# Optimization experiments

Measured on AMD Instinct MI355X. Metric: run time of the kernel, lower is better.

Reference implementation:

```python
import math
import jax, jax.numpy as jnp
import numpy as np

B, S, E, H = 4, 2048, 1024, 16
D = E // H


def setup_inputs() -> dict:
    key = jax.random.key(0)
    k1, k2, k3 = jax.random.split(key, 3)
    return {
        "hidden_state": jax.random.normal(k1, (B, S, E), dtype=jnp.float32),
        "attention_mask": jnp.zeros((B, 1, 1, S), dtype=jnp.float32),
        "W_attn": jax.random.normal(k2, (E, 3 * E), dtype=jnp.float32) * 0.02,
        "b_attn": jnp.zeros((3 * E,), dtype=jnp.float32),
        "W_proj": jax.random.normal(k3, (E, E), dtype=jnp.float32) * 0.02,
        "b_proj": jnp.zeros((E,), dtype=jnp.float32),
    }


def reference(hidden_state, attention_mask, W_attn, b_attn, W_proj, b_proj):
    b, s, e = hidden_state.shape
    d = e // H
    # c_attn (HF Conv1D): x @ W + b -> [B,S,3E]
    x = hidden_state @ W_attn + b_attn
    q, k, v = jnp.split(x, 3, axis=-1)
    # split heads -> [B,H,S,D]
    q = q.reshape(b, s, H, d).transpose(0, 2, 1, 3)
    k = k.reshape(b, s, H, d).transpose(0, 2, 1, 3)
    v = v.reshape(b, s, H, d).transpose(0, 2, 1, 3)
    # scores [B,H,S,S]; scale=True divides by sqrt(d_head)
    w = jnp.einsum("bhqd,bhkd->bhqk", q, k) / math.sqrt(d)
    causal = jnp.tril(jnp.ones((s, s), dtype=w.dtype))[None, None]
    w = w * causal + (-10000.0) * (1.0 - causal)
    w = w + attention_mask
    w = jax.nn.softmax(w, axis=-1)  # attn_dropout p=0 (eval)
    out = jnp.einsum("bhqk,bhkd->bhqd", w, v)
    # merge heads -> [B,S,E]
    out = out.transpose(0, 2, 1, 3).reshape(b, s, e)
    # c_proj; resid_dropout p=0 (eval)
    return out @ W_proj + b_proj
```

## Files before the change

kernel.cpp:

```cpp
#include <hip/hip_runtime.h>
#include <hip/hip_bf16.h>

typedef __attribute__((ext_vector_type(4))) float f32x4;
typedef __attribute__((ext_vector_type(8))) short bf16x8;

#define B_SZ  4
#define S_LEN 2048
#define EMB   1024
#define NH    16
#define DH    64
#define E3    3072
#define QKLD  2048
#define LOG2E 1.4426950408889634f
#define SC2   (0.125f * LOG2E)
#define MSTAT 14.0f

#define VMCNT(N) asm volatile("s_waitcnt vmcnt(" #N ")" ::: "memory")
#define RAWBAR() asm volatile("s_barrier" ::: "memory")

__device__ __forceinline__ void gload_lds16(const void* g, void* l) {
  __builtin_amdgcn_global_load_lds((const __attribute__((address_space(1))) void*)g,
                                   (__attribute__((address_space(3))) void*)l, 16, 0, 0);
}

__device__ __forceinline__ float bf2f(unsigned short u) {
  union { unsigned int i; float f; } c;
  c.i = (unsigned int)u << 16;
  return c.f;
}

__device__ __forceinline__ unsigned pack_bf16_rtz(float hi, float lo) {
  union { float f; unsigned u; } a, b;
  a.f = hi; b.f = lo;
  return (a.u & 0xffff0000u) | (b.u >> 16);
}

__global__ void cvt_bf16_kernel(const float* __restrict__ in,
                                __hip_bfloat16* __restrict__ out, int n) {
  const int i = (blockIdx.x * 256 + threadIdx.x) * 4;
  if (i >= n) return;
  const float4 v = *(const float4*)(in + i);
  __align__(8) __hip_bfloat16 o[4];
  o[0] = __float2bfloat16(v.x); o[1] = __float2bfloat16(v.y);
  o[2] = __float2bfloat16(v.z); o[3] = __float2bfloat16(v.w);
  *(uint2*)(out + i) = *(const uint2*)o;
}

__global__ __launch_bounds__(256)
void transpose_cvt(const float* __restrict__ in, __hip_bfloat16* __restrict__ out,
                   int R, int C) {
  __shared__ float tile[32][33];
  const int tx = threadIdx.x & 31, ty = threadIdx.x >> 5;
  const int c = blockIdx.x * 32 + tx;
#pragma unroll
  for (int i = 0; i < 32; i += 8)
    tile[ty + i][tx] = in[(size_t)(blockIdx.y * 32 + ty + i) * C + c];
  __syncthreads();
  const int r2 = blockIdx.y * 32 + tx;
#pragma unroll
  for (int i = 0; i < 32; i += 8)
    out[(size_t)(blockIdx.x * 32 + ty + i) * R + r2] = __float2bfloat16(tile[tx][ty + i]);
}

template <int EPI>
__global__ __launch_bounds__(256, 2)
void gemm_v4(const __hip_bfloat16* __restrict__ A, const __hip_bfloat16* __restrict__ BT,
             const float* __restrict__ bias, void* __restrict__ Cout,
             __hip_bfloat16* __restrict__ vt) {
  __shared__ __attribute__((aligned(16))) char lds[73728];
  const int tid = threadIdx.x;
  const int lane = tid & 63, w = tid >> 6;
  const int lr = lane & 15, lg = lane >> 4, lg4 = lg * 4;
  const int wm = w >> 1, wn = w & 1;

  const int j = blockIdx.x;
  const int g = (j & 7) * ((int)gridDim.x >> 3) + (j >> 3);
  const int bx = g & 63, by = g >> 6;
  const int m0 = bx * 128, n0 = by * 256;

  const int ar1 = tid >> 2;
  const int ar2 = ar1 + 64;
  const int cg = tid & 3;
  const int ac1 = (cg ^ ((ar1 >> 1) & 3)) * 8;
  const int ac2 = (cg ^ ((ar2 >> 1) & 3)) * 8;
  const __hip_bfloat16* pa1 = A + (size_t)(m0 + ar1) * 1024 + ac1;
  const __hip_bfloat16* pa2 = A + (size_t)(m0 + ar2) * 1024 + ac2;
  const int br0 = tid >> 2, br1 = br0 + 64, br2 = br0 + 128, br3 = br0 + 192;
  const __hip_bfloat16* pb0 = BT + (size_t)(n0 + br0) * 1024 + (cg ^ ((br0 >> 1) & 3)) * 8;
  const __hip_bfloat16* pb1 = BT + (size_t)(n0 + br1) * 1024 + (cg ^ ((br1 >> 1) & 3)) * 8;
  const __hip_bfloat16* pb2 = BT + (size_t)(n0 + br2) * 1024 + (cg ^ ((br2 >> 1) & 3)) * 8;
  const __hip_bfloat16* pb3 = BT + (size_t)(n0 + br3) * 1024 + (cg ^ ((br3 >> 1) & 3)) * 8;
  char* const dA1 = lds + tid * 16;
  char* const dA2 = lds + 4096 + tid * 16;
  char* const dB0 = lds + 8192 + tid * 16;
  char* const dB1 = lds + 8192 + 4096 + tid * 16;
  char* const dB2 = lds + 8192 + 8192 + tid * 16;
  char* const dB3 = lds + 8192 + 12288 + tid * 16;

#define STG_V4(BUF, T) { \
    const int off_ = (T) * 32; \
    gload_lds16(pa1 + off_, dA1 + (BUF) * 24576); \
    gload_lds16(pa2 + off_, dA2 + (BUF) * 24576); \
    gload_lds16(pb0 + off_, dB0 + (BUF) * 24576); \
    gload_lds16(pb1 + off_, dB1 + (BUF) * 24576); \
    gload_lds16(pb2 + off_, dB2 + (BUF) * 24576); \
    gload_lds16(pb3 + off_, dB3 + (BUF) * 24576); }

  const int sw = (lg ^ ((lr >> 1) & 3)) << 4;
  const int abyte = (wm * 64 + lr) * 64 + sw;
  const int bbyte = 8192 + (wn * 128 + lr) * 64 + sw;

  f32x4 acc[4][8] = {};

  STG_V4(0, 0); STG_V4(1, 1);

  int cur = 0;
#pragma unroll 1
  for (int t = 0; t < 32; ++t) {
    if (t < 31) { VMCNT(6); } else { VMCNT(0); }
    RAWBAR();
    if (t + 2 < 32) {
      const int nb = (cur >= 1) ? cur - 1 : 2;
      STG_V4(nb, t + 2);
    }
    const char* base = lds + cur * 24576;
    bf16x8 a[4], b[8];
#pragma unroll
    for (int m = 0; m < 4; ++m) a[m] = *(const bf16x8*)(base + abyte + m * 1024);
#pragma unroll
    for (int n = 0; n < 8; ++n) b[n] = *(const bf16x8*)(base + bbyte + n * 1024);
#pragma unroll
    for (int m = 0; m < 4; ++m)
#pragma unroll
      for (int n = 0; n < 8; ++n)
        acc[m][n] = __builtin_amdgcn_mfma_f32_16x16x32_bf16(a[m], b[n], acc[m][n], 0, 0, 0);
    cur = (cur == 2) ? 0 : cur + 1;
  }

  if (EPI == 0 && n0 >= 2 * EMB) {
#pragma unroll
    for (int m = 0; m < 4; ++m) {
      const int rowg0 = m0 + wm * 64 + m * 16 + lg4;
      const int bz = rowg0 >> 11, sloc = rowg0 & (S_LEN - 1);
#pragma unroll
      for (int n = 0; n < 8; ++n) {
        const int col = n0 + wn * 128 + n * 16 + lr;
        const int c2 = col - 2 * EMB;
        const int hh = c2 >> 6, dd = c2 & 63;
        const float bv = bias[col];
        __align__(8) __hip_bfloat16 pb[4];
#pragma unroll
        for (int r = 0; r < 4; ++r) pb[r] = __float2bfloat16(acc[m][n][r] + bv);
        *(uint2*)&vt[(size_t)((bz * NH + hh) * DH + dd) * S_LEN + sloc] = *(const uint2*)pb;
      }
    }
  } else if (EPI == 0) {
#pragma unroll
    for (int m = 0; m < 4; ++m) {
#pragma unroll
      for (int n = 0; n < 8; ++n) {
        const int col = n0 + wn * 128 + n * 16 + lr;
        const float bv = bias[col];
#pragma unroll
        for (int r = 0; r < 4; ++r) {
          const int rowg = m0 + wm * 64 + m * 16 + lg4 + r;
          ((__hip_bfloat16*)Cout)[(size_t)rowg * QKLD + col] = __float2bfloat16(acc[m][n][r] + bv);
        }
      }
    }
  } else {
#pragma unroll
    for (int m = 0; m < 4; ++m) {
#pragma unroll
      for (int n = 0; n < 8; ++n) {
        const int col = n0 + wn * 128 + n * 16 + lr;
        const float bv = bias[col];
#pragma unroll
        for (int r = 0; r < 4; ++r) {
          const int rowg = m0 + wm * 64 + m * 16 + lg4 + r;
          ((float*)Cout)[(size_t)rowg * EMB + col] = acc[m][n][r] + bv;
        }
      }
    }
  }
#undef STG_V4
}

template <bool DIAG>
__device__ __forceinline__ void qstep(const char* Ks, const char* Vs,
                                      __hip_bfloat16 (*Psw)[72], const __hip_bfloat16* Msb,
                                      int msoff, const bf16x8 (&aq)[2], f32x4 (&acc)[4],
                                      float& lrun, int lr, int lg, int lg4, int wq) {
  f32x4 sacc[4] = {};
  __builtin_amdgcn_s_setprio(1);
#pragma unroll
  for (int kt = 0; kt < 4; ++kt)
#pragma unroll
    for (int ks = 0; ks < 2; ++ks) {
      const bf16x8 kb = *(const bf16x8*)(Ks + (kt * 16 + lr) * 128 +
                                         (((ks * 4 + lg) ^ (lr & 7)) << 4));
      sacc[kt] = __builtin_amdgcn_mfma_f32_16x16x32_bf16(kb, aq[ks], sacc[kt], 0, 0, 0);
    }
  __builtin_amdgcn_s_setprio(0);
#pragma unroll
  for (int kt = 0; kt < 4; ++kt) {
    const ushort4 mb = *(const ushort4*)&Msb[msoff + kt * 16 + lg4];
    float pp[4];
#pragma unroll
    for (int r = 0; r < 4; ++r) {
      float sv = sacc[kt][r] * SC2 + bf2f(((const unsigned short*)&mb)[r]);
      if (DIAG && (kt * 16 + lg4 + r > wq)) sv = -1.0e9f;
      pp[r] = __builtin_amdgcn_exp2f(sv);
    }
    lrun += (pp[0] + pp[1]) + (pp[2] + pp[3]);
    uint2 uu;
    uu.x = pack_bf16_rtz(pp[1], pp[0]);
    uu.y = pack_bf16_rtz(pp[3], pp[2]);
    *(uint2*)&Psw[lr][kt * 16 + lg4] = uu;
  }
#pragma unroll
  for (int ks = 0; ks < 2; ++ks) {
    const bf16x8 pa = *(const bf16x8*)&Psw[lr][ks * 32 + lg * 8];
    __builtin_amdgcn_s_setprio(1);
#pragma unroll
    for (int dt = 0; dt < 4; ++dt) {
      const bf16x8 vb = *(const bf16x8*)(Vs + (dt * 16 + lr) * 128 +
                                         (((ks * 4 + lg) ^ (lr & 7)) << 4));
      acc[dt] = __builtin_amdgcn_mfma_f32_16x16x32_bf16(pa, vb, acc[dt], 0, 0, 0);
    }
    __builtin_amdgcn_s_setprio(0);
  }
}

template <bool DIAGA>
__device__ __forceinline__ void qstep2(const char* Ks, const char* Vs,
                                       __hip_bfloat16 (*PsA)[72], __hip_bfloat16 (*PsB)[72],
                                       const __hip_bfloat16* Msb, int msoff,
                                       const bf16x8 (&aqA)[2], const bf16x8 (&aqB)[2],
                                       f32x4 (&accA)[4], f32x4 (&accB)[4],
                                       float& lA, float& lB, int lr, int lg, int lg4, int wq) {
  f32x4 sA[4] = {}, sB[4] = {};
  __builtin_amdgcn_s_setprio(1);
#pragma unroll
  for (int kt = 0; kt < 4; ++kt)
#pragma unroll
    for (int ks = 0; ks < 2; ++ks) {
      const bf16x8 kb = *(const bf16x8*)(Ks + (kt * 16 + lr) * 128 +
                                         (((ks * 4 + lg) ^ (lr & 7)) << 4));
      sA[kt] = __builtin_amdgcn_mfma_f32_16x16x32_bf16(kb, aqA[ks], sA[kt], 0, 0, 0);
      sB[kt] = __builtin_amdgcn_mfma_f32_16x16x32_bf16(kb, aqB[ks], sB[kt], 0, 0, 0);
    }
  __builtin_amdgcn_s_setprio(0);
#pragma unroll
  for (int kt = 0; kt < 4; ++kt) {
    const ushort4 mb = *(const ushort4*)&Msb[msoff + kt * 16 + lg4];
    float pA[4], pB[4];
#pragma unroll
    for (int r = 0; r < 4; ++r) {
      const float mkr = bf2f(((const unsigned short*)&mb)[r]);
      float svA = sA[kt][r] * SC2 + mkr;
      if (DIAGA && (kt * 16 + lg4 + r > wq)) svA = -1.0e9f;
      const float svB = sB[kt][r] * SC2 + mkr;
      pA[r] = __builtin_amdgcn_exp2f(svA);
      pB[r] = __builtin_amdgcn_exp2f(svB);
    }
    lA += (pA[0] + pA[1]) + (pA[2] + pA[3]);
    lB += (pB[0] + pB[1]) + (pB[2] + pB[3]);
    uint2 ua, ub;
    ua.x = pack_bf16_rtz(pA[1], pA[0]);
    ua.y = pack_bf16_rtz(pA[3], pA[2]);
    ub.x = pack_bf16_rtz(pB[1], pB[0]);
    ub.y = pack_bf16_rtz(pB[3], pB[2]);
    *(uint2*)&PsA[lr][kt * 16 + lg4] = ua;
    *(uint2*)&PsB[lr][kt * 16 + lg4] = ub;
  }
#pragma unroll
  for (int ks = 0; ks < 2; ++ks) {
    const bf16x8 paA = *(const bf16x8*)&PsA[lr][ks * 32 + lg * 8];
    const bf16x8 paB = *(const bf16x8*)&PsB[lr][ks * 32 + lg * 8];
    __builtin_amdgcn_s_setprio(1);
#pragma unroll
    for (int dt = 0; dt < 4; ++dt) {
      const bf16x8 vb = *(const bf16x8*)(Vs + (dt * 16 + lr) * 128 +
                                         (((ks * 4 + lg) ^ (lr & 7)) << 4));
      accA[dt] = __builtin_amdgcn_mfma_f32_16x16x32_bf16(paA, vb, accA[dt], 0, 0, 0);
      accB[dt] = __builtin_amdgcn_mfma_f32_16x16x32_bf16(paB, vb, accB[dt], 0, 0, 0);
    }
    __builtin_amdgcn_s_setprio(0);
  }
}

#define STAGE_LOAD_BUMP()                                                          \
  {                                                                                \
    kpre[0] = *(const bf16x8*)kcur;                                                \
    kpre[1] = *(const bf16x8*)(kcur + 8 * QKLD);                                   \
    vpre[0] = *(const bf16x8*)vcur;                                                \
    vpre[1] = *(const bf16x8*)(vcur + 8 * S_LEN);                                  \
    kcur += 64 * QKLD;                                                             \
    vcur += 64;                                                                    \
  }

#define TILE_SYNC(PREFETCH)                                                        \
  {                                                                                \
    __syncthreads();                                                               \
    *(bf16x8*)kw0 = kpre[0];                                                       \
    *(bf16x8*)(kw0 + 1024) = kpre[1];                                              \
    *(bf16x8*)vw0 = vpre[0];                                                       \
    *(bf16x8*)(vw0 + 1024) = vpre[1];                                              \
    __syncthreads();                                                               \
    if (PREFETCH) STAGE_LOAD_BUMP();                                               \
  }

__global__ __launch_bounds__(256, 4)
void flash_attn10(const __hip_bfloat16* __restrict__ qk, const __hip_bfloat16* __restrict__ vt,
                  const float* __restrict__ amask, __hip_bfloat16* __restrict__ aout) {
  const int j = blockIdx.x;
  const int g = (j & 7) + 8 * (j >> 7);
  const int x = (((j >> 3) & 15) + (((j >> 8) & 3) << 2)) & 15;
  const int h = g >> 2, bz = g & 3;

  const int tid = threadIdx.x;
  const int lane = tid & 63, w = tid >> 6;
  const int lr = lane & 15, lg = lane >> 4, lg4 = lg * 4;
  const int wq = w * 16 + lr;

  const int qta = x, qtb = 31 - x;

  __shared__ __align__(16) __hip_bfloat16 Ks[64 * 64];
  __shared__ __align__(16) __hip_bfloat16 Vs[64 * 64];
  __shared__ __align__(16) __hip_bfloat16 Ps[4][2][16][72];
  __shared__ __align__(8)  __hip_bfloat16 Msb[S_LEN];

  {
    const int e = tid * 8;
    const f32x4 m0v = *(const f32x4*)&amask[bz * S_LEN + e];
    const f32x4 m1v = *(const f32x4*)&amask[bz * S_LEN + e + 4];
    __align__(16) __hip_bfloat16 mb[8];
#pragma unroll
    for (int jj = 0; jj < 4; ++jj) {
      mb[jj]     = __float2bfloat16(m0v[jj] * LOG2E - MSTAT);
      mb[jj + 4] = __float2bfloat16(m1v[jj] * LOG2E - MSTAT);
    }
    *(uint4*)&Msb[e] = *(const uint4*)mb;
  }

  bf16x8 aqA[2], aqB[2];
  {
    const __hip_bfloat16* qpA =
        qk + (size_t)(bz * S_LEN + qta * 64 + w * 16 + lr) * QKLD + h * DH + lg * 8;
    aqA[0] = *(const bf16x8*)qpA; aqA[1] = *(const bf16x8*)(qpA + 32);
    const __hip_bfloat16* qpB =
        qk + (size_t)(bz * S_LEN + qtb * 64 + w * 16 + lr) * QKLD + h * DH + lg * 8;
    aqB[0] = *(const bf16x8*)qpB; aqB[1] = *(const bf16x8*)(qpB + 32);
  }

  f32x4 accA[4] = {}, accB[4] = {};
  float lA = 0.f, lB = 0.f;

  const __hip_bfloat16* kcur = qk + (size_t)bz * S_LEN * QKLD + EMB + h * DH +
                               (size_t)(w * 16 + (lane >> 3)) * QKLD + (lane & 7) * 8;
  const __hip_bfloat16* vcur = vt + (size_t)((bz * NH + h) * DH + w * 16 + (lane >> 3)) * S_LEN +
                               (lane & 7) * 8;
  char* kw0 = (char*)Ks + (w * 16 + (lane >> 3)) * 128 + (((lane & 7) ^ (lane >> 3)) << 4);
  char* vw0 = (char*)Vs + (w * 16 + (lane >> 3)) * 128 + (((lane & 7) ^ (lane >> 3)) << 4);

  bf16x8 kpre[2], vpre[2];
  STAGE_LOAD_BUMP();

  int msoff = 0;
  for (int t = 0; t < qta; ++t) {
    TILE_SYNC(true);
    qstep2<false>((char*)Ks, (char*)Vs, Ps[w][0], Ps[w][1], Msb, msoff,
                  aqA, aqB, accA, accB, lA, lB, lr, lg, lg4, wq);
    msoff += 64;
  }
  TILE_SYNC(true);
  qstep2<true>((char*)Ks, (char*)Vs, Ps[w][0], Ps[w][1], Msb, msoff,
               aqA, aqB, accA, accB, lA, lB, lr, lg, lg4, wq);
  msoff += 64;
  for (int t = qta + 1; t < qtb; ++t) {
    TILE_SYNC(true);
    qstep<false>((char*)Ks, (char*)Vs, Ps[w][1], Msb, msoff, aqB, accB, lB, lr, lg, lg4, wq);
    msoff += 64;
  }
  TILE_SYNC(false);
  qstep<true>((char*)Ks, (char*)Vs, Ps[w][1], Msb, msoff, aqB, accB, lB, lr, lg, lg4, wq);

  lA += __shfl_xor(lA, 16); lA += __shfl_xor(lA, 32);
  lB += __shfl_xor(lB, 16); lB += __shfl_xor(lB, 32);
  float lqA[4], lqB[4];
#pragma unroll
  for (int r = 0; r < 4; ++r) {
    lqA[r] = __shfl(lA, lg4 + r);
    lqB[r] = __shfl(lB, lg4 + r);
  }
#pragma unroll
  for (int dt = 0; dt < 4; ++dt)
#pragma unroll
    for (int r = 0; r < 4; ++r) {
      const int qA = qta * 64 + w * 16 + lg4 + r;
      aout[(size_t)(bz * S_LEN + qA) * EMB + h * DH + dt * 16 + lr] =
          __float2bfloat16(accA[dt][r] / lqA[r]);
      const int qB = qtb * 64 + w * 16 + lg4 + r;
      aout[(size_t)(bz * S_LEN + qB) * EMB + h * DH + dt * 16 + lr] =
          __float2bfloat16(accB[dt][r] / lqB[r]);
    }
}

extern "C" void kernel_launch(void* const* d_in, const int* in_sizes, int n_in,
                              void* d_out, int out_size, void* d_ws, size_t ws_size,
                              hipStream_t stream) {
  const float* hidden = (const float*)d_in[0];
  const float* amask  = (const float*)d_in[1];
  const float* W_attn = (const float*)d_in[2];
  const float* b_attn = (const float*)d_in[3];
  const float* W_proj = (const float*)d_in[4];
  const float* b_proj = (const float*)d_in[5];
  float* out = (float*)d_out;

  char* ws = (char*)d_ws;
  __hip_bfloat16* hbf   = (__hip_bfloat16*)(ws);
  __hip_bfloat16* WaT   = (__hip_bfloat16*)(ws + 16777216);
  __hip_bfloat16* WpT   = (__hip_bfloat16*)(ws + 23068672);
  __hip_bfloat16* qkQK  = (__hip_bfloat16*)(ws + 25165824);
  __hip_bfloat16* vt    = (__hip_bfloat16*)(ws + 58720256);
  __hip_bfloat16* aoutb = (__hip_bfloat16*)(ws + 75497472);

  cvt_bf16_kernel<<<dim3(8192), dim3(256), 0, stream>>>(hidden, hbf, B_SZ * S_LEN * EMB);
  transpose_cvt<<<dim3(96, 32), dim3(256), 0, stream>>>(W_attn, WaT, EMB, E3);
  transpose_cvt<<<dim3(32, 32), dim3(256), 0, stream>>>(W_proj, WpT, EMB, EMB);
  gemm_v4<0><<<dim3(768), dim3(256), 0, stream>>>(hbf, WaT, b_attn, qkQK, vt);
  flash_attn10<<<dim3(1024), dim3(256), 0, stream>>>(qkQK, vt, amask, aoutb);
  gemm_v4<1><<<dim3(256), dim3(256), 0, stream>>>(aoutb, WpT, b_proj, out, nullptr);
}
```

Measured before the change: 172.8 us.

## Use 128x384 tiles with double-buffered pipeline for QKV projection GEMM

Splits the templated GEMM into a dedicated QKV kernel and a projection kernel. The QKV kernel moves from 128x256 tiles (768 blocks, triple-buffered, two stages in flight) to 128x384 tiles (512 blocks, double-buffered, one stage in flight with a full vmcnt(0) wait each iteration). Each block now writes both the QK rows and the transposed V output per column tile. Larger tiles raise arithmetic intensity and shrink the grid to a multiple of the CU count, but they use more accumulator registers (48 f32x4 per thread) and the shallower prefetch exposes more load latency.

```diff
diff --git a/kernel.cpp b/kernel.cpp
--- a/kernel.cpp
+++ b/kernel.cpp
@@ -62,11 +62,93 @@
     out[(size_t)(blockIdx.x * 32 + ty + i) * R + r2] = __float2bfloat16(tile[tx][ty + i]);
 }
 
-template <int EPI>
 __global__ __launch_bounds__(256, 2)
-void gemm_v4(const __hip_bfloat16* __restrict__ A, const __hip_bfloat16* __restrict__ BT,
-             const float* __restrict__ bias, void* __restrict__ Cout,
-             __hip_bfloat16* __restrict__ vt) {
+void gemm_qkv_v5(const __hip_bfloat16* __restrict__ A, const __hip_bfloat16* __restrict__ BT,
+                 const float* __restrict__ bias, __hip_bfloat16* __restrict__ qkOut,
+                 __hip_bfloat16* __restrict__ vt) {
+  __shared__ __attribute__((aligned(16))) char lds[65536];
+  const int tid = threadIdx.x;
+  const int lane = tid & 63, w = tid >> 6;
+  const int lr = lane & 15, lg = lane >> 4, lg4 = lg * 4;
+  const int wm = w >> 1, wn = w & 1;
+
+  const int j = blockIdx.x;
+  const int g = (j & 7) * 64 + (j >> 3);
+  const int m0 = (g >> 3) * 128;
+  const int n0 = (g & 7) * 384;
+
+  const int r0 = tid >> 2, cg = tid & 3;
+  const int sc = (cg ^ ((r0 >> 1) & 3)) * 8;
+  const __hip_bfloat16* pA0 = A + (size_t)(m0 + r0) * 1024 + sc;
+  const __hip_bfloat16* pB0 = BT + (size_t)(n0 + r0) * 1024 + sc;
+  char* const dst = lds + tid * 16;
+
+#define STG5(B, T) { \
+    const int o_ = (T) * 32; \
+    gload_lds16(pA0 + o_,           dst + (B) * 32768); \
+    gload_lds16(pA0 + 65536 + o_,   dst + (B) * 32768 + 4096); \
+    _Pragma("unroll") \
+    for (int i_ = 0; i_ < 6; ++i_) \
+      gload_lds16(pB0 + i_ * 65536 + o_, dst + (B) * 32768 + 8192 + i_ * 4096); }
+
+  const int sw = (lg ^ ((lr >> 1) & 3)) << 4;
+  const int abyte = (wm * 64 + lr) * 64 + sw;
+  const int bbyte = 8192 + (wn * 192 + lr) * 64 + sw;
+
+  f32x4 acc[4][12] = {};
+
+  STG5(0, 0);
+  VMCNT(0);
+  RAWBAR();
+
+  int cur = 0;
+#pragma unroll 1
+  for (int t = 0; t < 32; ++t) {
+    if (t < 31) STG5(cur ^ 1, t + 1);
+    const char* base = lds + cur * 32768;
+    bf16x8 a[4], b[12];
+#pragma unroll
+    for (int m = 0; m < 4; ++m) a[m] = *(const bf16x8*)(base + abyte + m * 1024);
+#pragma unroll
+    for (int n = 0; n < 12; ++n) b[n] = *(const bf16x8*)(base + bbyte + n * 1024);
+#pragma unroll
+    for (int m = 0; m < 4; ++m)
+#pragma unroll
+      for (int n = 0; n < 12; ++n)
+        acc[m][n] = __builtin_amdgcn_mfma_f32_16x16x32_bf16(a[m], b[n], acc[m][n], 0, 0, 0);
+    if (t < 31) { VMCNT(0); RAWBAR(); }
+    cur ^= 1;
+  }
+
+#pragma unroll
+  for (int m = 0; m < 4; ++m) {
+    const int rowg0 = m0 + wm * 64 + m * 16 + lg4;
+    const int bz = rowg0 >> 11, sloc = rowg0 & (S_LEN - 1);
+#pragma unroll
+    for (int n = 0; n < 12; ++n) {
+      const int colb = n0 + wn * 192 + n * 16;
+      const int col = colb + lr;
+      const float bv = bias[col];
+      if (colb < 2 * EMB) {
+#pragma unroll
+        for (int r = 0; r < 4; ++r)
+          qkOut[(size_t)(rowg0 + r) * QKLD + col] = __float2bfloat16(acc[m][n][r] + bv);
+      } else {
+        const int c2 = col - 2 * EMB;
+        const int hh = c2 >> 6, dd = c2 & 63;
+        __align__(8) __hip_bfloat16 pb[4];
+#pragma unroll
+        for (int r = 0; r < 4; ++r) pb[r] = __float2bfloat16(acc[m][n][r] + bv);
+        *(uint2*)&vt[(size_t)((bz * NH + hh) * DH + dd) * S_LEN + sloc] = *(const uint2*)pb;
+      }
+    }
+  }
+#undef STG5
+}
+
+__global__ __launch_bounds__(256, 2)
+void gemm_proj_v4(const __hip_bfloat16* __restrict__ A, const __hip_bfloat16* __restrict__ BT,
+                  const float* __restrict__ bias, float* __restrict__ Cout) {
   __shared__ __attribute__((aligned(16))) char lds[73728];
   const int tid = threadIdx.x;
   const int lane = tid & 63, w = tid >> 6;
@@ -82,29 +164,20 @@
   const int ar2 = ar1 + 64;
   const int cg = tid & 3;
   const int ac1 = (cg ^ ((ar1 >> 1) & 3)) * 8;
-  const int ac2 = (cg ^ ((ar2 >> 1) & 3)) * 8;
   const __hip_bfloat16* pa1 = A + (size_t)(m0 + ar1) * 1024 + ac1;
-  const __hip_bfloat16* pa2 = A + (size_t)(m0 + ar2) * 1024 + ac2;
-  const int br0 = tid >> 2, br1 = br0 + 64, br2 = br0 + 128, br3 = br0 + 192;
-  const __hip_bfloat16* pb0 = BT + (size_t)(n0 + br0) * 1024 + (cg ^ ((br0 >> 1) & 3)) * 8;
-  const __hip_bfloat16* pb1 = BT + (size_t)(n0 + br1) * 1024 + (cg ^ ((br1 >> 1) & 3)) * 8;
-  const __hip_bfloat16* pb2 = BT + (size_t)(n0 + br2) * 1024 + (cg ^ ((br2 >> 1) & 3)) * 8;
-  const __hip_bfloat16* pb3 = BT + (size_t)(n0 + br3) * 1024 + (cg ^ ((br3 >> 1) & 3)) * 8;
+  const __hip_bfloat16* pa2 = A + (size_t)(m0 + ar2) * 1024 + ac1;
+  const __hip_bfloat16* pb0 = BT + (size_t)(n0 + ar1) * 1024 + ac1;
   char* const dA1 = lds + tid * 16;
   char* const dA2 = lds + 4096 + tid * 16;
   char* const dB0 = lds + 8192 + tid * 16;
-  char* const dB1 = lds + 8192 + 4096 + tid * 16;
-  char* const dB2 = lds + 8192 + 8192 + tid * 16;
-  char* const dB3 = lds + 8192 + 12288 + tid * 16;
-
-#define STG_V4(BUF, T) { \
+
+#define STG_P(BUF, T) { \
     const int off_ = (T) * 32; \
     gload_lds16(pa1 + off_, dA1 + (BUF) * 24576); \
     gload_lds16(pa2 + off_, dA2 + (BUF) * 24576); \
-    gload_lds16(pb0 + off_, dB0 + (BUF) * 24576); \
-    gload_lds16(pb1 + off_, dB1 + (BUF) * 24576); \
-    gload_lds16(pb2 + off_, dB2 + (BUF) * 24576); \
-    gload_lds16(pb3 + off_, dB3 + (BUF) * 24576); }
+    _Pragma("unroll") \
+    for (int i_ = 0; i_ < 4; ++i_) \
+      gload_lds16(pb0 + i_ * 65536 + off_, dB0 + (BUF) * 24576 + i_ * 4096); }
 
   const int sw = (lg ^ ((lr >> 1) & 3)) << 4;
   const int abyte = (wm * 64 + lr) * 64 + sw;
@@ -112,7 +185,7 @@
 
   f32x4 acc[4][8] = {};
 
-  STG_V4(0, 0); STG_V4(1, 1);
+  STG_P(0, 0); STG_P(1, 1);
 
   int cur = 0;
 #pragma unroll 1
@@ -121,7 +194,7 @@
     RAWBAR();
     if (t + 2 < 32) {
       const int nb = (cur >= 1) ? cur - 1 : 2;
-      STG_V4(nb, t + 2);
+      STG_P(nb, t + 2);
     }
     const char* base = lds + cur * 24576;
     bf16x8 a[4], b[8];
@@ -137,53 +210,20 @@
     cur = (cur == 2) ? 0 : cur + 1;
   }
 
-  if (EPI == 0 && n0 >= 2 * EMB) {
-#pragma unroll
-    for (int m = 0; m < 4; ++m) {
-      const int rowg0 = m0 + wm * 64 + m * 16 + lg4;
-      const int bz = rowg0 >> 11, sloc = rowg0 & (S_LEN - 1);
-#pragma unroll
-      for (int n = 0; n < 8; ++n) {
-        const int col = n0 + wn * 128 + n * 16 + lr;
-        const int c2 = col - 2 * EMB;
-        const int hh = c2 >> 6, dd = c2 & 63;
-        const float bv = bias[col];
-        __align__(8) __hip_bfloat16 pb[4];
-#pragma unroll
-        for (int r = 0; r < 4; ++r) pb[r] = __float2bfloat16(acc[m][n][r] + bv);
-        *(uint2*)&vt[(size_t)((bz * NH + hh) * DH + dd) * S_LEN + sloc] = *(const uint2*)pb;
+#pragma unroll
+  for (int m = 0; m < 4; ++m) {
+#pragma unroll
+    for (int n = 0; n < 8; ++n) {
+      const int col = n0 + wn * 128 + n * 16 + lr;
+      const float bv = bias[col];
+#pragma unroll
+      for (int r = 0; r < 4; ++r) {
+        const int rowg = m0 + wm * 64 + m * 16 + lg4 + r;
+        Cout[(size_t)rowg * EMB + col] = acc[m][n][r] + bv;
       }
     }
-  } else if (EPI == 0) {
-#pragma unroll
-    for (int m = 0; m < 4; ++m) {
-#pragma unroll
-      for (int n = 0; n < 8; ++n) {
-        const int col = n0 + wn * 128 + n * 16 + lr;
-        const float bv = bias[col];
-#pragma unroll
-        for (int r = 0; r < 4; ++r) {
-          const int rowg = m0 + wm * 64 + m * 16 + lg4 + r;
-          ((__hip_bfloat16*)Cout)[(size_t)rowg * QKLD + col] = __float2bfloat16(acc[m][n][r] + bv);
-        }
-      }
-    }
-  } else {
-#pragma unroll
-    for (int m = 0; m < 4; ++m) {
-#pragma unroll
-      for (int n = 0; n < 8; ++n) {
-        const int col = n0 + wn * 128 + n * 16 + lr;
-        const float bv = bias[col];
-#pragma unroll
-        for (int r = 0; r < 4; ++r) {
-          const int rowg = m0 + wm * 64 + m * 16 + lg4 + r;
-          ((float*)Cout)[(size_t)rowg * EMB + col] = acc[m][n][r] + bv;
-        }
-      }
-    }
-  }
-#undef STG_V4
+  }
+#undef STG_P
 }
 
 template <bool DIAG>
@@ -429,7 +469,7 @@
   cvt_bf16_kernel<<<dim3(8192), dim3(256), 0, stream>>>(hidden, hbf, B_SZ * S_LEN * EMB);
   transpose_cvt<<<dim3(96, 32), dim3(256), 0, stream>>>(W_attn, WaT, EMB, E3);
   transpose_cvt<<<dim3(32, 32), dim3(256), 0, stream>>>(W_proj, WpT, EMB, EMB);
-  gemm_v4<0><<<dim3(768), dim3(256), 0, stream>>>(hbf, WaT, b_attn, qkQK, vt);
+  gemm_qkv_v5<<<dim3(512), dim3(256), 0, stream>>>(hbf, WaT, b_attn, qkQK, vt);
   flash_attn10<<<dim3(1024), dim3(256), 0, stream>>>(qkQK, vt, amask, aoutb);
-  gemm_v4<1><<<dim3(256), dim3(256), 0, stream>>>(aoutb, WpT, b_proj, out, nullptr);
-}
+  gemm_proj_v4<<<dim3(256), dim3(256), 0, stream>>>(aoutb, WpT, b_proj, out);
+}
```

Measured after the change: 168.9 us (median of 2 runs). 2.2% less time.
